# Optimization experiments

Hardware: AMD Instinct MI355X
Metric: run time of the kernel (lower is better)

Reference implementation:

```python
import jax, jax.numpy as jnp
import numpy as np

NUM_STREAMS = 4
DIM = 256
SINKHORN_ITERS = 10
SINKHORN_TAU = 0.05


def sinkhorn_log(logits, num_iters=SINKHORN_ITERS, tau=SINKHORN_TAU):
    n = logits.shape[-1]
    z = logits / tau
    log_marginal = -jnp.log(jnp.asarray(float(n), dtype=logits.dtype))

    def body(carry, _):
        u, v = carry
        u = log_marginal - jax.scipy.special.logsumexp(z + v[None, :], axis=1)
        v = log_marginal - jax.scipy.special.logsumexp(z + u[:, None], axis=0)
        return (u, v), None

    u0 = jnp.zeros((n,), dtype=z.dtype)
    v0 = jnp.zeros((n,), dtype=z.dtype)
    (u, v), _ = jax.lax.scan(body, (u0, v0), None, length=num_iters)
    return jnp.exp(z + u[:, None] + v[None, :]) * n


def setup_inputs() -> dict:
    key = jax.random.key(0)
    k_res, k_w = jax.random.split(key)
    B = 65536
    residuals = jax.random.normal(k_res, (B, NUM_STREAMS, DIM), dtype=jnp.float32)
    # h_res_logits: -8 everywhere, 0 on diagonal (as in __init__)
    h_res_logits = jnp.full((NUM_STREAMS, NUM_STREAMS), -8.0, dtype=jnp.float32)
    h_res_logits = h_res_logits.at[jnp.arange(NUM_STREAMS), jnp.arange(NUM_STREAMS)].set(0.0)
    # h_pre_logits: -8 everywhere, 0 at init_residual_index=0
    h_pre_logits = jnp.full((NUM_STREAMS,), -8.0, dtype=jnp.float32).at[0].set(0.0)
    h_post_logits = jnp.zeros((NUM_STREAMS,), dtype=jnp.float32)
    # branch Linear(dim, dim, bias=False): weight (out, in), y = x @ W.T
    bound = 1.0 / np.sqrt(DIM)
    W_branch = jax.random.uniform(k_w, (DIM, DIM), dtype=jnp.float32, minval=-bound, maxval=bound)
    return {
        "residuals": residuals,
        "h_res_logits": h_res_logits,
        "h_pre_logits": h_pre_logits,
        "h_post_logits": h_post_logits,
        "W_branch": W_branch,
    }


def reference(residuals, h_res_logits, h_pre_logits, h_post_logits, W_branch):
    # residuals: (B, S, D)
    h_res = sinkhorn_log(h_res_logits)                     # (S, S) doubly-stochastic * n
    h_pre = jax.nn.softmax(h_pre_logits)                   # (S,)
    h_post = jax.nn.softmax(h_post_logits)                 # (S,)
    residuals_mixed = jnp.einsum('st,bsd->btd', h_res, residuals)
    branch_input = jnp.einsum('s,bsd->bd', h_pre, residuals)
    branch_output = branch_input @ W_branch.T              # (B, D)
    depth_out = jnp.einsum('bd,s->bsd', branch_output, h_post)
    return residuals_mixed + depth_out
```

## Files before the change

### kernel.cpp

```cpp
#include <hip/hip_runtime.h>

#define NSTREAMS 4
#define DIM 256
#define BM 16
#define NTHREADS 1024
#define TILES 16

typedef __attribute__((ext_vector_type(8))) short short8;
typedef __attribute__((ext_vector_type(4))) float f32x4;

static __device__ __forceinline__ int2 f2bf4(float4 v) {
    unsigned int lo, hi;
    asm("v_cvt_pk_bf16_f32 %0, %1, %2" : "=v"(lo) : "v"(v.x), "v"(v.y));
    asm("v_cvt_pk_bf16_f32 %0, %1, %2" : "=v"(hi) : "v"(v.z), "v"(v.w));
    int2 r; r.x = (int)lo; r.y = (int)hi;
    return r;
}

static __device__ __forceinline__ float rfl(float x) {
    int i = __builtin_amdgcn_readfirstlane(__builtin_bit_cast(int, x));
    return __builtin_bit_cast(float, i);
}

static __device__ __forceinline__ void barrier_lgkm() {
    asm volatile("s_waitcnt lgkmcnt(0)\n\ts_barrier" ::: "memory");
}

__global__ __launch_bounds__(NTHREADS, 1) void fused_kernel(
    const float* __restrict__ res,
    const float* __restrict__ Wb,
    const float* __restrict__ hres_l,
    const float* __restrict__ hpre_l,
    const float* __restrict__ hpost_l,
    float* __restrict__ out)
{
    __shared__ __align__(16) short bi_lds[2][BM][DIM + 8];

    const int t  = threadIdx.x;
    const int w  = t >> 6;
    const int l  = t & 63;
    const int lr = l & 15;
    const int lk = l >> 4;

    const long tile0 = (long)blockIdx.x * TILES;
    const long tstride = (long)BM * (NSTREAMS * DIM);
    const int d0 = w * 16 + lk * 4;
    const int dcol = w * 16 + lr;
    const float* rbase = res + (tile0 * BM + lr) * (NSTREAMS * DIM) + d0;

    float4 A0, A1, A2, A3;
    A0 = *reinterpret_cast<const float4*>(rbase + 0 * DIM);
    A1 = *reinterpret_cast<const float4*>(rbase + 1 * DIM);
    A2 = *reinterpret_cast<const float4*>(rbase + 2 * DIM);
    A3 = *reinterpret_cast<const float4*>(rbase + 3 * DIM);

    const float4* wrow4 = reinterpret_cast<const float4*>(Wb + dcol * DIM);
    float4 wfa[8], wfb[8];
    #pragma unroll
    for (int kk = 0; kk < 8; ++kk) {
        wfa[kk] = wrow4[kk * 8 + lk * 2];
        wfb[kk] = wrow4[kk * 8 + lk * 2 + 1];
    }

    float hres[4][4];
    float hp0, hp1, hp2, hp3;
    float hq[4];
    {
        const int li = l & 15;
        float z = hres_l[li] * 20.0f;
        float uu = 0.f, vv = 0.f;
        const float logm = -logf(4.0f);
        #pragma unroll 1
        for (int it = 0; it < 10; ++it) {
            float tj = z + vv;
            float m = fmaxf(tj, __shfl_xor(tj, 1));
            m = fmaxf(m, __shfl_xor(m, 2));
            float e = expf(tj - m);
            float ss = e + __shfl_xor(e, 1);
            ss += __shfl_xor(ss, 2);
            uu = logm - (m + logf(ss));
            float ti2 = z + uu;
            float m2 = fmaxf(ti2, __shfl_xor(ti2, 4));
            m2 = fmaxf(m2, __shfl_xor(m2, 8));
            float e2 = expf(ti2 - m2);
            float s2 = e2 + __shfl_xor(e2, 4);
            s2 += __shfl_xor(s2, 8);
            vv = logm - (m2 + logf(s2));
        }
        float hval = expf(z + uu + vv) * 4.0f;
        #pragma unroll
        for (int s = 0; s < 4; ++s)
            #pragma unroll
            for (int tt = 0; tt < 4; ++tt)
                hres[s][tt] = rfl(__shfl(hval, s * 4 + tt));
        float p0 = hpre_l[0], p1 = hpre_l[1], p2 = hpre_l[2], p3 = hpre_l[3];
        float pm = fmaxf(fmaxf(p0, p1), fmaxf(p2, p3));
        float e0 = expf(p0 - pm), e1 = expf(p1 - pm), e2 = expf(p2 - pm), e3 = expf(p3 - pm);
        float es = e0 + e1 + e2 + e3;
        hp0 = rfl(e0 / es); hp1 = rfl(e1 / es); hp2 = rfl(e2 / es); hp3 = rfl(e3 / es);
        float q0 = hpost_l[0], q1 = hpost_l[1], q2 = hpost_l[2], q3 = hpost_l[3];
        float qm = fmaxf(fmaxf(q0, q1), fmaxf(q2, q3));
        float f0 = expf(q0 - qm), f1 = expf(q1 - qm), f2 = expf(q2 - qm), f3 = expf(q3 - qm);
        float fs = f0 + f1 + f2 + f3;
        hq[0] = rfl(f0 / fs); hq[1] = rfl(f1 / fs); hq[2] = rfl(f2 / fs); hq[3] = rfl(f3 / fs);
    }

    short8 wf[8];
    #pragma unroll
    for (int kk = 0; kk < 8; ++kk) {
        union { int4 i; short8 s; } u8;
        int2 lo = f2bf4(wfa[kk]);
        int2 hi = f2bf4(wfb[kk]);
        u8.i.x = lo.x; u8.i.y = lo.y; u8.i.z = hi.x; u8.i.w = hi.y;
        wf[kk] = u8.s;
    }

    float4 opart[4];
    {
        float4 bi;
        bi.x = hp0 * A0.x + hp1 * A1.x + hp2 * A2.x + hp3 * A3.x;
        bi.y = hp0 * A0.y + hp1 * A1.y + hp2 * A2.y + hp3 * A3.y;
        bi.z = hp0 * A0.z + hp1 * A1.z + hp2 * A2.z + hp3 * A3.z;
        bi.w = hp0 * A0.w + hp1 * A1.w + hp2 * A2.w + hp3 * A3.w;
        *reinterpret_cast<int2*>(&bi_lds[0][lr][d0]) = f2bf4(bi);
        #pragma unroll
        for (int tt = 0; tt < 4; ++tt) {
            opart[tt].x = hres[0][tt] * A0.x + hres[1][tt] * A1.x + hres[2][tt] * A2.x + hres[3][tt] * A3.x;
            opart[tt].y = hres[0][tt] * A0.y + hres[1][tt] * A1.y + hres[2][tt] * A2.y + hres[3][tt] * A3.y;
            opart[tt].z = hres[0][tt] * A0.z + hres[1][tt] * A1.z + hres[2][tt] * A2.z + hres[3][tt] * A3.z;
            opart[tt].w = hres[0][tt] * A0.w + hres[1][tt] * A1.w + hres[2][tt] * A2.w + hres[3][tt] * A3.w;
        }
    }

    float4 B0, B1, B2, B3;
    B0 = *reinterpret_cast<const float4*>(rbase + tstride + 0 * DIM);
    B1 = *reinterpret_cast<const float4*>(rbase + tstride + 1 * DIM);
    B2 = *reinterpret_cast<const float4*>(rbase + tstride + 2 * DIM);
    B3 = *reinterpret_cast<const float4*>(rbase + tstride + 3 * DIM);

    barrier_lgkm();

    for (int ti = 0; ti < TILES; ti += 2) {
        {
            if (ti + 2 < TILES) {
                const float* rb = rbase + (ti + 2) * tstride;
                A0 = *reinterpret_cast<const float4*>(rb + 0 * DIM);
                A1 = *reinterpret_cast<const float4*>(rb + 1 * DIM);
                A2 = *reinterpret_cast<const float4*>(rb + 2 * DIM);
                A3 = *reinterpret_cast<const float4*>(rb + 3 * DIM);
            }
            __builtin_amdgcn_sched_barrier(0);
            f32x4 acc = {0.f, 0.f, 0.f, 0.f};
            #pragma unroll
            for (int kk = 0; kk < 8; ++kk) {
                short8 bfrag = *reinterpret_cast<const short8*>(&bi_lds[0][lr][kk * 32 + lk * 8]);
                acc = __builtin_amdgcn_mfma_f32_16x16x32_bf16(wf[kk], bfrag, acc, 0, 0, 0);
            }
            {
                float* obase = out + (((tile0 + ti) * BM + lr) * 4) * DIM + d0;
                #pragma unroll
                for (int tt = 0; tt < 4; ++tt) {
                    float4 o;
                    o.x = opart[tt].x + hq[tt] * acc[0];
                    o.y = opart[tt].y + hq[tt] * acc[1];
                    o.z = opart[tt].z + hq[tt] * acc[2];
                    o.w = opart[tt].w + hq[tt] * acc[3];
                    *reinterpret_cast<float4*>(obase + tt * DIM) = o;
                }
            }
            {
                float4 bi;
                bi.x = hp0 * B0.x + hp1 * B1.x + hp2 * B2.x + hp3 * B3.x;
                bi.y = hp0 * B0.y + hp1 * B1.y + hp2 * B2.y + hp3 * B3.y;
                bi.z = hp0 * B0.z + hp1 * B1.z + hp2 * B2.z + hp3 * B3.z;
                bi.w = hp0 * B0.w + hp1 * B1.w + hp2 * B2.w + hp3 * B3.w;
                *reinterpret_cast<int2*>(&bi_lds[1][lr][d0]) = f2bf4(bi);
                #pragma unroll
                for (int tt = 0; tt < 4; ++tt) {
                    opart[tt].x = hres[0][tt] * B0.x + hres[1][tt] * B1.x + hres[2][tt] * B2.x + hres[3][tt] * B3.x;
                    opart[tt].y = hres[0][tt] * B0.y + hres[1][tt] * B1.y + hres[2][tt] * B2.y + hres[3][tt] * B3.y;
                    opart[tt].z = hres[0][tt] * B0.z + hres[1][tt] * B1.z + hres[2][tt] * B2.z + hres[3][tt] * B3.z;
                    opart[tt].w = hres[0][tt] * B0.w + hres[1][tt] * B1.w + hres[2][tt] * B2.w + hres[3][tt] * B3.w;
                }
            }
            barrier_lgkm();
        }
        {
            if (ti + 3 < TILES) {
                const float* rb = rbase + (ti + 3) * tstride;
                B0 = *reinterpret_cast<const float4*>(rb + 0 * DIM);
                B1 = *reinterpret_cast<const float4*>(rb + 1 * DIM);
                B2 = *reinterpret_cast<const float4*>(rb + 2 * DIM);
                B3 = *reinterpret_cast<const float4*>(rb + 3 * DIM);
            }
            __builtin_amdgcn_sched_barrier(0);
            f32x4 acc = {0.f, 0.f, 0.f, 0.f};
            #pragma unroll
            for (int kk = 0; kk < 8; ++kk) {
                short8 bfrag = *reinterpret_cast<const short8*>(&bi_lds[1][lr][kk * 32 + lk * 8]);
                acc = __builtin_amdgcn_mfma_f32_16x16x32_bf16(wf[kk], bfrag, acc, 0, 0, 0);
            }
            {
                float* obase = out + (((tile0 + ti + 1) * BM + lr) * 4) * DIM + d0;
                #pragma unroll
                for (int tt = 0; tt < 4; ++tt) {
                    float4 o;
                    o.x = opart[tt].x + hq[tt] * acc[0];
                    o.y = opart[tt].y + hq[tt] * acc[1];
                    o.z = opart[tt].z + hq[tt] * acc[2];
                    o.w = opart[tt].w + hq[tt] * acc[3];
                    *reinterpret_cast<float4*>(obase + tt * DIM) = o;
                }
            }
            if (ti + 2 < TILES) {
                float4 bi;
                bi.x = hp0 * A0.x + hp1 * A1.x + hp2 * A2.x + hp3 * A3.x;
                bi.y = hp0 * A0.y + hp1 * A1.y + hp2 * A2.y + hp3 * A3.y;
                bi.z = hp0 * A0.z + hp1 * A1.z + hp2 * A2.z + hp3 * A3.z;
                bi.w = hp0 * A0.w + hp1 * A1.w + hp2 * A2.w + hp3 * A3.w;
                *reinterpret_cast<int2*>(&bi_lds[0][lr][d0]) = f2bf4(bi);
                #pragma unroll
                for (int tt = 0; tt < 4; ++tt) {
                    opart[tt].x = hres[0][tt] * A0.x + hres[1][tt] * A1.x + hres[2][tt] * A2.x + hres[3][tt] * A3.x;
                    opart[tt].y = hres[0][tt] * A0.y + hres[1][tt] * A1.y + hres[2][tt] * A2.y + hres[3][tt] * A3.y;
                    opart[tt].z = hres[0][tt] * A0.z + hres[1][tt] * A1.z + hres[2][tt] * A2.z + hres[3][tt] * A3.z;
                    opart[tt].w = hres[0][tt] * A0.w + hres[1][tt] * A1.w + hres[2][tt] * A2.w + hres[3][tt] * A3.w;
                }
            }
            barrier_lgkm();
        }
    }
}

extern "C" void kernel_launch(void* const* d_in, const int* in_sizes, int n_in,
                              void* d_out, int out_size, void* d_ws, size_t ws_size,
                              hipStream_t stream) {
    const float* res     = (const float*)d_in[0];
    const float* hres_l  = (const float*)d_in[1];
    const float* hpre_l  = (const float*)d_in[2];
    const float* hpost_l = (const float*)d_in[3];
    const float* Wb      = (const float*)d_in[4];
    float* out = (float*)d_out;

    const int Btot = in_sizes[0] / (NSTREAMS * DIM);
    const int grid = Btot / (BM * TILES);

    fused_kernel<<<grid, NTHREADS, 0, stream>>>(
        res, Wb, hres_l, hpre_l, hpost_l, out);
}
```

Baseline: 119.9 us.

## Process tile pairs per barrier with quad-buffered LDS and paired prefetch

Restructures the main loop so each iteration prefetches two tiles at once, computes and stores two tiles, then stages the next two tiles' branch inputs into a quad-buffered LDS region. This halves the number of block-wide barriers and issues more global loads in flight per iteration. The cost is more live registers (two sets of partial outputs and prefetched data) and double the LDS footprint.

Result: slower. 128.9 us (+7.5%).

```diff
diff --git a/kernel.cpp b/kernel.cpp
--- a/kernel.cpp
+++ b/kernel.cpp
@@ -34,7 +34,7 @@
     const float* __restrict__ hpost_l,
     float* __restrict__ out)
 {
-    __shared__ __align__(16) short bi_lds[2][BM][DIM + 8];
+    __shared__ __align__(16) short bi_lds[4][BM][DIM + 8];
 
     const int t  = threadIdx.x;
     const int w  = t >> 6;
@@ -48,11 +48,15 @@
     const int dcol = w * 16 + lr;
     const float* rbase = res + (tile0 * BM + lr) * (NSTREAMS * DIM) + d0;
 
-    float4 A0, A1, A2, A3;
+    float4 A0, A1, A2, A3, B0, B1, B2, B3;
     A0 = *reinterpret_cast<const float4*>(rbase + 0 * DIM);
     A1 = *reinterpret_cast<const float4*>(rbase + 1 * DIM);
     A2 = *reinterpret_cast<const float4*>(rbase + 2 * DIM);
     A3 = *reinterpret_cast<const float4*>(rbase + 3 * DIM);
+    B0 = *reinterpret_cast<const float4*>(rbase + tstride + 0 * DIM);
+    B1 = *reinterpret_cast<const float4*>(rbase + tstride + 1 * DIM);
+    B2 = *reinterpret_cast<const float4*>(rbase + tstride + 2 * DIM);
+    B3 = *reinterpret_cast<const float4*>(rbase + tstride + 3 * DIM);
 
     const float4* wrow4 = reinterpret_cast<const float4*>(Wb + dcol * DIM);
     float4 wfa[8], wfb[8];
@@ -115,7 +119,7 @@
         wf[kk] = u8.s;
     }
 
-    float4 opart[4];
+    float4 opA[4], opB[4];
     {
         float4 bi;
         bi.x = hp0 * A0.x + hp1 * A1.x + hp2 * A2.x + hp3 * A3.x;
@@ -125,47 +129,98 @@
         *reinterpret_cast<int2*>(&bi_lds[0][lr][d0]) = f2bf4(bi);
         #pragma unroll
         for (int tt = 0; tt < 4; ++tt) {
-            opart[tt].x = hres[0][tt] * A0.x + hres[1][tt] * A1.x + hres[2][tt] * A2.x + hres[3][tt] * A3.x;
-            opart[tt].y = hres[0][tt] * A0.y + hres[1][tt] * A1.y + hres[2][tt] * A2.y + hres[3][tt] * A3.y;
-            opart[tt].z = hres[0][tt] * A0.z + hres[1][tt] * A1.z + hres[2][tt] * A2.z + hres[3][tt] * A3.z;
-            opart[tt].w = hres[0][tt] * A0.w + hres[1][tt] * A1.w + hres[2][tt] * A2.w + hres[3][tt] * A3.w;
-        }
-    }
-
-    float4 B0, B1, B2, B3;
-    B0 = *reinterpret_cast<const float4*>(rbase + tstride + 0 * DIM);
-    B1 = *reinterpret_cast<const float4*>(rbase + tstride + 1 * DIM);
-    B2 = *reinterpret_cast<const float4*>(rbase + tstride + 2 * DIM);
-    B3 = *reinterpret_cast<const float4*>(rbase + tstride + 3 * DIM);
-
+            opA[tt].x = hres[0][tt] * A0.x + hres[1][tt] * A1.x + hres[2][tt] * A2.x + hres[3][tt] * A3.x;
+            opA[tt].y = hres[0][tt] * A0.y + hres[1][tt] * A1.y + hres[2][tt] * A2.y + hres[3][tt] * A3.y;
+            opA[tt].z = hres[0][tt] * A0.z + hres[1][tt] * A1.z + hres[2][tt] * A2.z + hres[3][tt] * A3.z;
+            opA[tt].w = hres[0][tt] * A0.w + hres[1][tt] * A1.w + hres[2][tt] * A2.w + hres[3][tt] * A3.w;
+        }
+    }
+    {
+        float4 bi;
+        bi.x = hp0 * B0.x + hp1 * B1.x + hp2 * B2.x + hp3 * B3.x;
+        bi.y = hp0 * B0.y + hp1 * B1.y + hp2 * B2.y + hp3 * B3.y;
+        bi.z = hp0 * B0.z + hp1 * B1.z + hp2 * B2.z + hp3 * B3.z;
+        bi.w = hp0 * B0.w + hp1 * B1.w + hp2 * B2.w + hp3 * B3.w;
+        *reinterpret_cast<int2*>(&bi_lds[1][lr][d0]) = f2bf4(bi);
+        #pragma unroll
+        for (int tt = 0; tt < 4; ++tt) {
+            opB[tt].x = hres[0][tt] * B0.x + hres[1][tt] * B1.x + hres[2][tt] * B2.x + hres[3][tt] * B3.x;
+            opB[tt].y = hres[0][tt] * B0.y + hres[1][tt] * B1.y + hres[2][tt] * B2.y + hres[3][tt] * B3.y;
+            opB[tt].z = hres[0][tt] * B0.z + hres[1][tt] * B1.z + hres[2][tt] * B2.z + hres[3][tt] * B3.z;
+            opB[tt].w = hres[0][tt] * B0.w + hres[1][tt] * B1.w + hres[2][tt] * B2.w + hres[3][tt] * B3.w;
+        }
+    }
     barrier_lgkm();
 
     for (int ti = 0; ti < TILES; ti += 2) {
+        const int pb = (ti >> 1) & 1;
+        const bool more = (ti + 2 < TILES);
+        if (more) {
+            const float* ra = rbase + (ti + 2) * tstride;
+            A0 = *reinterpret_cast<const float4*>(ra + 0 * DIM);
+            A1 = *reinterpret_cast<const float4*>(ra + 1 * DIM);
+            A2 = *reinterpret_cast<const float4*>(ra + 2 * DIM);
+            A3 = *reinterpret_cast<const float4*>(ra + 3 * DIM);
+            const float* rb = rbase + (ti + 3) * tstride;
+            B0 = *reinterpret_cast<const float4*>(rb + 0 * DIM);
+            B1 = *reinterpret_cast<const float4*>(rb + 1 * DIM);
+            B2 = *reinterpret_cast<const float4*>(rb + 2 * DIM);
+            B3 = *reinterpret_cast<const float4*>(rb + 3 * DIM);
+        }
+        __builtin_amdgcn_sched_barrier(0);
+
         {
-            if (ti + 2 < TILES) {
-                const float* rb = rbase + (ti + 2) * tstride;
-                A0 = *reinterpret_cast<const float4*>(rb + 0 * DIM);
-                A1 = *reinterpret_cast<const float4*>(rb + 1 * DIM);
-                A2 = *reinterpret_cast<const float4*>(rb + 2 * DIM);
-                A3 = *reinterpret_cast<const float4*>(rb + 3 * DIM);
-            }
-            __builtin_amdgcn_sched_barrier(0);
             f32x4 acc = {0.f, 0.f, 0.f, 0.f};
             #pragma unroll
             for (int kk = 0; kk < 8; ++kk) {
-                short8 bfrag = *reinterpret_cast<const short8*>(&bi_lds[0][lr][kk * 32 + lk * 8]);
+                short8 bfrag = *reinterpret_cast<const short8*>(&bi_lds[2 * pb][lr][kk * 32 + lk * 8]);
                 acc = __builtin_amdgcn_mfma_f32_16x16x32_bf16(wf[kk], bfrag, acc, 0, 0, 0);
             }
+            float* obase = out + (((tile0 + ti) * BM + lr) * 4) * DIM + d0;
+            #pragma unroll
+            for (int tt = 0; tt < 4; ++tt) {
+                float4 o;
+                o.x = opA[tt].x + hq[tt] * acc[0];
+                o.y = opA[tt].y + hq[tt] * acc[1];
+                o.z = opA[tt].z + hq[tt] * acc[2];
+                o.w = opA[tt].w + hq[tt] * acc[3];
+                *reinterpret_cast<float4*>(obase + tt * DIM) = o;
+            }
+        }
+        {
+            f32x4 acc = {0.f, 0.f, 0.f, 0.f};
+            #pragma unroll
+            for (int kk = 0; kk < 8; ++kk) {
+                short8 bfrag = *reinterpret_cast<const short8*>(&bi_lds[2 * pb + 1][lr][kk * 32 + lk * 8]);
+                acc = __builtin_amdgcn_mfma_f32_16x16x32_bf16(wf[kk], bfrag, acc, 0, 0, 0);
+            }
+            float* obase = out + (((tile0 + ti + 1) * BM + lr) * 4) * DIM + d0;
+            #pragma unroll
+            for (int tt = 0; tt < 4; ++tt) {
+                float4 o;
+                o.x = opB[tt].x + hq[tt] * acc[0];
+                o.y = opB[tt].y + hq[tt] * acc[1];
+                o.z = opB[tt].z + hq[tt] * acc[2];
+                o.w = opB[tt].w + hq[tt] * acc[3];
+                *reinterpret_cast<float4*>(obase + tt * DIM) = o;
+            }
+        }
+
+        if (more) {
+            const int q = 2 * (pb ^ 1);
             {
-                float* obase = out + (((tile0 + ti) * BM + lr) * 4) * DIM + d0;
+                float4 bi;
+                bi.x = hp0 * A0.x + hp1 * A1.x + hp2 * A2.x + hp3 * A3.x;
+                bi.y = hp0 * A0.y + hp1 * A1.y + hp2 * A2.y + hp3 * A3.y;
+                bi.z = hp0 * A0.z + hp1 * A1.z + hp2 * A2.z + hp3 * A3.z;
+                bi.w = hp0 * A0.w + hp1 * A1.w + hp2 * A2.w + hp3 * A3.w;
+                *reinterpret_cast<int2*>(&bi_lds[q][lr][d0]) = f2bf4(bi);
                 #pragma unroll
                 for (int tt = 0; tt < 4; ++tt) {
-                    float4 o;
-                    o.x = opart[tt].x + hq[tt] * acc[0];
-                    o.y = opart[tt].y + hq[tt] * acc[1];
-                    o.z = opart[tt].z + hq[tt] * acc[2];
-                    o.w = opart[tt].w + hq[tt] * acc[3];
-                    *reinterpret_cast<float4*>(obase + tt * DIM) = o;
+                    opA[tt].x = hres[0][tt] * A0.x + hres[1][tt] * A1.x + hres[2][tt] * A2.x + hres[3][tt] * A3.x;
+                    opA[tt].y = hres[0][tt] * A0.y + hres[1][tt] * A1.y + hres[2][tt] * A2.y + hres[3][tt] * A3.y;
+                    opA[tt].z = hres[0][tt] * A0.z + hres[1][tt] * A1.z + hres[2][tt] * A2.z + hres[3][tt] * A3.z;
+                    opA[tt].w = hres[0][tt] * A0.w + hres[1][tt] * A1.w + hres[2][tt] * A2.w + hres[3][tt] * A3.w;
                 }
             }
             {
@@ -174,57 +229,13 @@
                 bi.y = hp0 * B0.y + hp1 * B1.y + hp2 * B2.y + hp3 * B3.y;
                 bi.z = hp0 * B0.z + hp1 * B1.z + hp2 * B2.z + hp3 * B3.z;
                 bi.w = hp0 * B0.w + hp1 * B1.w + hp2 * B2.w + hp3 * B3.w;
-                *reinterpret_cast<int2*>(&bi_lds[1][lr][d0]) = f2bf4(bi);
+                *reinterpret_cast<int2*>(&bi_lds[q + 1][lr][d0]) = f2bf4(bi);
                 #pragma unroll
                 for (int tt = 0; tt < 4; ++tt) {
-                    opart[tt].x = hres[0][tt] * B0.x + hres[1][tt] * B1.x + hres[2][tt] * B2.x + hres[3][tt] * B3.x;
-                    opart[tt].y = hres[0][tt] * B0.y + hres[1][tt] * B1.y + hres[2][tt] * B2.y + hres[3][tt] * B3.y;
-                    opart[tt].z = hres[0][tt] * B0.z + hres[1][tt] * B1.z + hres[2][tt] * B2.z + hres[3][tt] * B3.z;
-                    opart[tt].w = hres[0][tt] * B0.w + hres[1][tt] * B1.w + hres[2][tt] * B2.w + hres[3][tt] * B3.w;
-                }
-            }
-            barrier_lgkm();
-        }
-        {
-            if (ti + 3 < TILES) {
-                const float* rb = rbase + (ti + 3) * tstride;
-                B0 = *reinterpret_cast<const float4*>(rb + 0 * DIM);
-                B1 = *reinterpret_cast<const float4*>(rb + 1 * DIM);
-                B2 = *reinterpret_cast<const float4*>(rb + 2 * DIM);
-                B3 = *reinterpret_cast<const float4*>(rb + 3 * DIM);
-            }
-            __builtin_amdgcn_sched_barrier(0);
-            f32x4 acc = {0.f, 0.f, 0.f, 0.f};
-            #pragma unroll
-            for (int kk = 0; kk < 8; ++kk) {
-                short8 bfrag = *reinterpret_cast<const short8*>(&bi_lds[1][lr][kk * 32 + lk * 8]);
-                acc = __builtin_amdgcn_mfma_f32_16x16x32_bf16(wf[kk], bfrag, acc, 0, 0, 0);
-            }
-            {
-                float* obase = out + (((tile0 + ti + 1) * BM + lr) * 4) * DIM + d0;
-                #pragma unroll
-                for (int tt = 0; tt < 4; ++tt) {
-                    float4 o;
-                    o.x = opart[tt].x + hq[tt] * acc[0];
-                    o.y = opart[tt].y + hq[tt] * acc[1];
-                    o.z = opart[tt].z + hq[tt] * acc[2];
-                    o.w = opart[tt].w + hq[tt] * acc[3];
-                    *reinterpret_cast<float4*>(obase + tt * DIM) = o;
-                }
-            }
-            if (ti + 2 < TILES) {
-                float4 bi;
-                bi.x = hp0 * A0.x + hp1 * A1.x + hp2 * A2.x + hp3 * A3.x;
-                bi.y = hp0 * A0.y + hp1 * A1.y + hp2 * A2.y + hp3 * A3.y;
-                bi.z = hp0 * A0.z + hp1 * A1.z + hp2 * A2.z + hp3 * A3.z;
-                bi.w = hp0 * A0.w + hp1 * A1.w + hp2 * A2.w + hp3 * A3.w;
-                *reinterpret_cast<int2*>(&bi_lds[0][lr][d0]) = f2bf4(bi);
-                #pragma unroll
-                for (int tt = 0; tt < 4; ++tt) {
-                    opart[tt].x = hres[0][tt] * A0.x + hres[1][tt] * A1.x + hres[2][tt] * A2.x + hres[3][tt] * A3.x;
-                    opart[tt].y = hres[0][tt] * A0.y + hres[1][tt] * A1.y + hres[2][tt] * A2.y + hres[3][tt] * A3.y;
-                    opart[tt].z = hres[0][tt] * A0.z + hres[1][tt] * A1.z + hres[2][tt] * A2.z + hres[3][tt] * A3.z;
-                    opart[tt].w = hres[0][tt] * A0.w + hres[1][tt] * A1.w + hres[2][tt] * A2.w + hres[3][tt] * A3.w;
+                    opB[tt].x = hres[0][tt] * B0.x + hres[1][tt] * B1.x + hres[2][tt] * B2.x + hres[3][tt] * B3.x;
+                    opB[tt].y = hres[0][tt] * B0.y + hres[1][tt] * B1.y + hres[2][tt] * B2.y + hres[3][tt] * B3.y;
+                    opB[tt].z = hres[0][tt] * B0.z + hres[1][tt] * B1.z + hres[2][tt] * B2.z + hres[3][tt] * B3.z;
+                    opB[tt].w = hres[0][tt] * B0.w + hres[1][tt] * B1.w + hres[2][tt] * B2.w + hres[3][tt] * B3.w;
                 }
             }
             barrier_lgkm();
```

## Remap threads to row-contiguous loads and stores, transposing GEMM output via LDS

Applied to the files above, without the earlier changes.

Each wave now handles one batch row, and each lane loads a contiguous float4 across the full 256-wide row, so global loads and stores are fully contiguous per wave. Before, each wave spanned 16 rows with 64-byte segments. The MFMA accumulator is staged through a new fp32 LDS buffer and re-read in the row-contiguous layout before the epilogue. The residual-mix partials are now computed at store time instead of being precomputed and held in registers. This adds an extra LDS round-trip and barrier per tile, and the next-tile prefetch now issues after the stores rather than before the MFMAs.

Result: faster. 114.4 us, median of 3 (-4.6%).

```diff
diff --git a/kernel.cpp b/kernel.cpp
--- a/kernel.cpp
+++ b/kernel.cpp
@@ -35,6 +35,7 @@
     float* __restrict__ out)
 {
     __shared__ __align__(16) short bi_lds[2][BM][DIM + 8];
+    __shared__ __align__(16) float bo_lds[BM][DIM + 4];
 
     const int t  = threadIdx.x;
     const int w  = t >> 6;
@@ -44,15 +45,15 @@
 
     const long tile0 = (long)blockIdx.x * TILES;
     const long tstride = (long)BM * (NSTREAMS * DIM);
-    const int d0 = w * 16 + lk * 4;
+    const float* rl0 = res + (tile0 * BM + w) * (long)(NSTREAMS * DIM) + l * 4;
+    float* ob0 = out + (tile0 * BM + w) * (long)(4 * DIM) + l * 4;
     const int dcol = w * 16 + lr;
-    const float* rbase = res + (tile0 * BM + lr) * (NSTREAMS * DIM) + d0;
 
     float4 A0, A1, A2, A3;
-    A0 = *reinterpret_cast<const float4*>(rbase + 0 * DIM);
-    A1 = *reinterpret_cast<const float4*>(rbase + 1 * DIM);
-    A2 = *reinterpret_cast<const float4*>(rbase + 2 * DIM);
-    A3 = *reinterpret_cast<const float4*>(rbase + 3 * DIM);
+    A0 = *reinterpret_cast<const float4*>(rl0 + 0 * DIM);
+    A1 = *reinterpret_cast<const float4*>(rl0 + 1 * DIM);
+    A2 = *reinterpret_cast<const float4*>(rl0 + 2 * DIM);
+    A3 = *reinterpret_cast<const float4*>(rl0 + 3 * DIM);
 
     const float4* wrow4 = reinterpret_cast<const float4*>(Wb + dcol * DIM);
     float4 wfa[8], wfb[8];
@@ -115,117 +116,100 @@
         wf[kk] = u8.s;
     }
 
-    float4 opart[4];
     {
         float4 bi;
         bi.x = hp0 * A0.x + hp1 * A1.x + hp2 * A2.x + hp3 * A3.x;
         bi.y = hp0 * A0.y + hp1 * A1.y + hp2 * A2.y + hp3 * A3.y;
         bi.z = hp0 * A0.z + hp1 * A1.z + hp2 * A2.z + hp3 * A3.z;
         bi.w = hp0 * A0.w + hp1 * A1.w + hp2 * A2.w + hp3 * A3.w;
-        *reinterpret_cast<int2*>(&bi_lds[0][lr][d0]) = f2bf4(bi);
-        #pragma unroll
-        for (int tt = 0; tt < 4; ++tt) {
-            opart[tt].x = hres[0][tt] * A0.x + hres[1][tt] * A1.x + hres[2][tt] * A2.x + hres[3][tt] * A3.x;
-            opart[tt].y = hres[0][tt] * A0.y + hres[1][tt] * A1.y + hres[2][tt] * A2.y + hres[3][tt] * A3.y;
-            opart[tt].z = hres[0][tt] * A0.z + hres[1][tt] * A1.z + hres[2][tt] * A2.z + hres[3][tt] * A3.z;
-            opart[tt].w = hres[0][tt] * A0.w + hres[1][tt] * A1.w + hres[2][tt] * A2.w + hres[3][tt] * A3.w;
-        }
-    }
-
+        *reinterpret_cast<int2*>(&bi_lds[0][w][l * 4]) = f2bf4(bi);
+    }
     float4 B0, B1, B2, B3;
-    B0 = *reinterpret_cast<const float4*>(rbase + tstride + 0 * DIM);
-    B1 = *reinterpret_cast<const float4*>(rbase + tstride + 1 * DIM);
-    B2 = *reinterpret_cast<const float4*>(rbase + tstride + 2 * DIM);
-    B3 = *reinterpret_cast<const float4*>(rbase + tstride + 3 * DIM);
+    B0 = *reinterpret_cast<const float4*>(rl0 + tstride + 0 * DIM);
+    B1 = *reinterpret_cast<const float4*>(rl0 + tstride + 1 * DIM);
+    B2 = *reinterpret_cast<const float4*>(rl0 + tstride + 2 * DIM);
+    B3 = *reinterpret_cast<const float4*>(rl0 + tstride + 3 * DIM);
 
     barrier_lgkm();
 
     for (int ti = 0; ti < TILES; ti += 2) {
         {
-            if (ti + 2 < TILES) {
-                const float* rb = rbase + (ti + 2) * tstride;
-                A0 = *reinterpret_cast<const float4*>(rb + 0 * DIM);
-                A1 = *reinterpret_cast<const float4*>(rb + 1 * DIM);
-                A2 = *reinterpret_cast<const float4*>(rb + 2 * DIM);
-                A3 = *reinterpret_cast<const float4*>(rb + 3 * DIM);
-            }
-            __builtin_amdgcn_sched_barrier(0);
             f32x4 acc = {0.f, 0.f, 0.f, 0.f};
             #pragma unroll
             for (int kk = 0; kk < 8; ++kk) {
                 short8 bfrag = *reinterpret_cast<const short8*>(&bi_lds[0][lr][kk * 32 + lk * 8]);
                 acc = __builtin_amdgcn_mfma_f32_16x16x32_bf16(wf[kk], bfrag, acc, 0, 0, 0);
             }
+            *reinterpret_cast<f32x4*>(&bo_lds[lr][(w << 4) + (lk << 2)]) = acc;
+            barrier_lgkm();
             {
-                float* obase = out + (((tile0 + ti) * BM + lr) * 4) * DIM + d0;
+                f32x4 bo = *reinterpret_cast<const f32x4*>(&bo_lds[w][l * 4]);
+                float* ob = ob0 + ti * (long)(BM * 4 * DIM);
                 #pragma unroll
                 for (int tt = 0; tt < 4; ++tt) {
                     float4 o;
-                    o.x = opart[tt].x + hq[tt] * acc[0];
-                    o.y = opart[tt].y + hq[tt] * acc[1];
-                    o.z = opart[tt].z + hq[tt] * acc[2];
-                    o.w = opart[tt].w + hq[tt] * acc[3];
-                    *reinterpret_cast<float4*>(obase + tt * DIM) = o;
+                    o.x = hq[tt] * bo[0] + hres[0][tt] * A0.x + hres[1][tt] * A1.x + hres[2][tt] * A2.x + hres[3][tt] * A3.x;
+                    o.y = hq[tt] * bo[1] + hres[0][tt] * A0.y + hres[1][tt] * A1.y + hres[2][tt] * A2.y + hres[3][tt] * A3.y;
+                    o.z = hq[tt] * bo[2] + hres[0][tt] * A0.z + hres[1][tt] * A1.z + hres[2][tt] * A2.z + hres[3][tt] * A3.z;
+                    o.w = hq[tt] * bo[3] + hres[0][tt] * A0.w + hres[1][tt] * A1.w + hres[2][tt] * A2.w + hres[3][tt] * A3.w;
+                    *reinterpret_cast<float4*>(ob + tt * DIM) = o;
                 }
             }
+            if (ti + 2 < TILES) {
+                const float* rb = rl0 + (ti + 2) * tstride;
+                A0 = *reinterpret_cast<const float4*>(rb + 0 * DIM);
+                A1 = *reinterpret_cast<const float4*>(rb + 1 * DIM);
+                A2 = *reinterpret_cast<const float4*>(rb + 2 * DIM);
+                A3 = *reinterpret_cast<const float4*>(rb + 3 * DIM);
+            }
+            __builtin_amdgcn_sched_barrier(0);
             {
                 float4 bi;
                 bi.x = hp0 * B0.x + hp1 * B1.x + hp2 * B2.x + hp3 * B3.x;
                 bi.y = hp0 * B0.y + hp1 * B1.y + hp2 * B2.y + hp3 * B3.y;
                 bi.z = hp0 * B0.z + hp1 * B1.z + hp2 * B2.z + hp3 * B3.z;
                 bi.w = hp0 * B0.w + hp1 * B1.w + hp2 * B2.w + hp3 * B3.w;
-                *reinterpret_cast<int2*>(&bi_lds[1][lr][d0]) = f2bf4(bi);
-                #pragma unroll
-                for (int tt = 0; tt < 4; ++tt) {
-                    opart[tt].x = hres[0][tt] * B0.x + hres[1][tt] * B1.x + hres[2][tt] * B2.x + hres[3][tt] * B3.x;
-                    opart[tt].y = hres[0][tt] * B0.y + hres[1][tt] * B1.y + hres[2][tt] * B2.y + hres[3][tt] * B3.y;
-                    opart[tt].z = hres[0][tt] * B0.z + hres[1][tt] * B1.z + hres[2][tt] * B2.z + hres[3][tt] * B3.z;
-                    opart[tt].w = hres[0][tt] * B0.w + hres[1][tt] * B1.w + hres[2][tt] * B2.w + hres[3][tt] * B3.w;
-                }
+                *reinterpret_cast<int2*>(&bi_lds[1][w][l * 4]) = f2bf4(bi);
             }
             barrier_lgkm();
         }
         {
-            if (ti + 3 < TILES) {
-                const float* rb = rbase + (ti + 3) * tstride;
-                B0 = *reinterpret_cast<const float4*>(rb + 0 * DIM);
-                B1 = *reinterpret_cast<const float4*>(rb + 1 * DIM);
-                B2 = *reinterpret_cast<const float4*>(rb + 2 * DIM);
-                B3 = *reinterpret_cast<const float4*>(rb + 3 * DIM);
-            }
-            __builtin_amdgcn_sched_barrier(0);
             f32x4 acc = {0.f, 0.f, 0.f, 0.f};
             #pragma unroll
             for (int kk = 0; kk < 8; ++kk) {
                 short8 bfrag = *reinterpret_cast<const short8*>(&bi_lds[1][lr][kk * 32 + lk * 8]);
                 acc = __builtin_amdgcn_mfma_f32_16x16x32_bf16(wf[kk], bfrag, acc, 0, 0, 0);
             }
+            *reinterpret_cast<f32x4*>(&bo_lds[lr][(w << 4) + (lk << 2)]) = acc;
+            barrier_lgkm();
             {
-                float* obase = out + (((tile0 + ti + 1) * BM + lr) * 4) * DIM + d0;
+                f32x4 bo = *reinterpret_cast<const f32x4*>(&bo_lds[w][l * 4]);
+                float* ob = ob0 + (ti + 1) * (long)(BM * 4 * DIM);
                 #pragma unroll
                 for (int tt = 0; tt < 4; ++tt) {
                     float4 o;
-                    o.x = opart[tt].x + hq[tt] * acc[0];
-                    o.y = opart[tt].y + hq[tt] * acc[1];
-                    o.z = opart[tt].z + hq[tt] * acc[2];
-                    o.w = opart[tt].w + hq[tt] * acc[3];
-                    *reinterpret_cast<float4*>(obase + tt * DIM) = o;
+                    o.x = hq[tt] * bo[0] + hres[0][tt] * B0.x + hres[1][tt] * B1.x + hres[2][tt] * B2.x + hres[3][tt] * B3.x;
+                    o.y = hq[tt] * bo[1] + hres[0][tt] * B0.y + hres[1][tt] * B1.y + hres[2][tt] * B2.y + hres[3][tt] * B3.y;
+                    o.z = hq[tt] * bo[2] + hres[0][tt] * B0.z + hres[1][tt] * B1.z + hres[2][tt] * B2.z + hres[3][tt] * B3.z;
+                    o.w = hq[tt] * bo[3] + hres[0][tt] * B0.w + hres[1][tt] * B1.w + hres[2][tt] * B2.w + hres[3][tt] * B3.w;
+                    *reinterpret_cast<float4*>(ob + tt * DIM) = o;
                 }
             }
+            if (ti + 3 < TILES) {
+                const float* rb = rl0 + (ti + 3) * tstride;
+                B0 = *reinterpret_cast<const float4*>(rb + 0 * DIM);
+                B1 = *reinterpret_cast<const float4*>(rb + 1 * DIM);
+                B2 = *reinterpret_cast<const float4*>(rb + 2 * DIM);
+                B3 = *reinterpret_cast<const float4*>(rb + 3 * DIM);
+            }
+            __builtin_amdgcn_sched_barrier(0);
             if (ti + 2 < TILES) {
                 float4 bi;
                 bi.x = hp0 * A0.x + hp1 * A1.x + hp2 * A2.x + hp3 * A3.x;
                 bi.y = hp0 * A0.y + hp1 * A1.y + hp2 * A2.y + hp3 * A3.y;
                 bi.z = hp0 * A0.z + hp1 * A1.z + hp2 * A2.z + hp3 * A3.z;
                 bi.w = hp0 * A0.w + hp1 * A1.w + hp2 * A2.w + hp3 * A3.w;
-                *reinterpret_cast<int2*>(&bi_lds[0][lr][d0]) = f2bf4(bi);
-                #pragma unroll
-                for (int tt = 0; tt < 4; ++tt) {
-                    opart[tt].x = hres[0][tt] * A0.x + hres[1][tt] * A1.x + hres[2][tt] * A2.x + hres[3][tt] * A3.x;
-                    opart[tt].y = hres[0][tt] * A0.y + hres[1][tt] * A1.y + hres[2][tt] * A2.y + hres[3][tt] * A3.y;
-                    opart[tt].z = hres[0][tt] * A0.z + hres[1][tt] * A1.z + hres[2][tt] * A2.z + hres[3][tt] * A3.z;
-                    opart[tt].w = hres[0][tt] * A0.w + hres[1][tt] * A1.w + hres[2][tt] * A2.w + hres[3][tt] * A3.w;
-                }
+                *reinterpret_cast<int2*>(&bi_lds[0][w][l * 4]) = f2bf4(bi);
             }
             barrier_lgkm();
         }
```
